# Optimization experiments

Measured on AMD Instinct MI355X. Metric: run time of the kernel, lower is better.

Reference implementation:

```python
import jax, jax.numpy as jnp
import numpy as np

NUM_HEADS = 16
ROPE_BASE = 10000.0


def apply_rope(x):
    # x: [B, T, H, D]; torchtune-style interleaved-pair RoPE, positions 0..T-1
    B, T, H, D = x.shape
    inv_freq = 1.0 / (ROPE_BASE ** (jnp.arange(0, D, 2, dtype=jnp.float32) / D))  # [D/2]
    pos = jnp.arange(T, dtype=jnp.float32)
    freqs = pos[:, None] * inv_freq[None, :]              # [T, D/2]
    cos = jnp.cos(freqs)[None, :, None, :].astype(x.dtype)
    sin = jnp.sin(freqs)[None, :, None, :].astype(x.dtype)
    x1 = x[..., 0::2]
    x2 = x[..., 1::2]
    o1 = x1 * cos - x2 * sin
    o2 = x2 * cos + x1 * sin
    return jnp.stack([o1, o2], axis=-1).reshape(B, T, H, D)


def setup_inputs() -> dict:
    key = jax.random.key(0)
    k1, k2, k3 = jax.random.split(key, 3)
    B, T, C = 2, 8192, 1024
    x = jax.random.normal(k1, (B, T, C), dtype=jnp.float32)
    # torch Linear weight layout [out_features, in_features]; fan-in scaling
    Wqkv = jax.random.normal(k2, (3 * C, C), dtype=jnp.float32) * (C ** -0.5)
    Wout = jax.random.normal(k3, (C, C), dtype=jnp.float32) * (C ** -0.5)
    return {"x": x, "Wqkv": Wqkv, "Wout": Wout}


def reference(x, Wqkv, Wout):
    B, T, C = x.shape
    H = NUM_HEADS
    D = C // H
    qkv = (x @ Wqkv.T).reshape(B, T, 3, H, D)
    q, k, v = qkv[:, :, 0], qkv[:, :, 1], qkv[:, :, 2]   # each [B, T, H, D]
    q = apply_rope(q)
    k = apply_rope(k)
    # Faithful to source: SDPA is called on [B, T, H, D] WITHOUT transposing,
    # so torch attends over the heads axis (L = H) with (B, T) as batch dims.
    scale = 1.0 / jnp.sqrt(jnp.asarray(D, dtype=x.dtype))
    scores = jnp.einsum('btqd,btkd->btqk', q, k) * scale  # [B, T, H, H]
    attn = jax.nn.softmax(scores, axis=-1)
    out = jnp.einsum('btqk,btkd->btqd', attn, v)          # [B, T, H, D]
    # Replicate attn_output.transpose(1, 2).contiguous().view(B, T, C)
    out = out.transpose(0, 2, 1, 3).reshape(B, T, C)
    return out @ Wout.T
```

## Files before the change

kernel.cpp:

```cpp
#include <hip/hip_runtime.h>
#include <stdint.h>

#define TT 8192
#define BT 16384
#define MCH 8192

typedef __attribute__((ext_vector_type(8))) __bf16 bf16x8;
typedef __attribute__((ext_vector_type(4))) __bf16 bf16x4;
typedef __attribute__((ext_vector_type(4))) short short4v;
typedef __attribute__((ext_vector_type(4))) float floatx4;

__device__ __forceinline__ float bf2f(unsigned short h) {
  union { unsigned u; float f; } x; x.u = ((unsigned)h) << 16; return x.f;
}
__device__ __forceinline__ unsigned short f2bf(float f) {
  union { float f; unsigned u; } x; x.f = f;
  unsigned r = (x.u + 0x7fffu + ((x.u >> 16) & 1u)) >> 16;
  return (unsigned short)r;
}
__device__ __forceinline__ void async16(const void* g, void* l) {
  __builtin_amdgcn_global_load_lds(
      (__attribute__((address_space(1))) void*)g,
      (__attribute__((address_space(3))) void*)l, 16, 0, 0);
}

__global__ __launch_bounds__(256) void cvt_f2b(
    const float* __restrict__ src, unsigned short* __restrict__ dst, int n4) {
  const int i = blockIdx.x * 256 + threadIdx.x;
  if (i < n4) {
    const float4 f = ((const float4*)src)[i];
    union { uint2 u2; unsigned short s[4]; } o;
    o.s[0] = f2bf(f.x); o.s[1] = f2bf(f.y);
    o.s[2] = f2bf(f.z); o.s[3] = f2bf(f.w);
    ((uint2*)dst)[i] = o.u2;
  }
}

__global__ __launch_bounds__(256) void rope_table_k(float2* __restrict__ tab) {
  const int i = blockIdx.x * 256 + threadIdx.x;
  if (i < TT * 32) {
    const int t = i >> 5, p = i & 31;
    const float f = (float)t * exp2f((float)p * -0.41524101186092f);
    float s, c;
    sincosf(f, &s, &c);
    tab[i] = make_float2(c, s);
  }
}

template <bool CF32>
__global__ __launch_bounds__(512, 4) void gemm_k32(
    const unsigned short* __restrict__ A,
    const unsigned short* __restrict__ W,
    void* __restrict__ C,
    int M, int N, int K)
{
  __shared__ __align__(16) unsigned short sm[2][(256 + 128) * 32];

  const int tid  = threadIdx.x;
  const int lane = tid & 63;
  const int wid  = tid >> 6;
  const int wr   = wid >> 1;
  const int wc   = wid & 1;
  const int lm   = lane & 15;
  const int kg   = lane >> 4;
  const int cxor = (lm >> 1) & 3;

  const int nb  = N >> 7;
  const int cpx = (int)gridDim.x >> 3;
  const int bid = blockIdx.x;
  const int swz = (bid & 7) * cpx + (bid >> 3);
  const int bm  = swz / nb;
  const int bn  = swz % nb;

  const int NT = K >> 5;

  const int sr  = lane >> 2;
  const int scb = lane & 3;
  const unsigned short* gsrc0;
  const unsigned short* gsrc1;
  const unsigned short* gsrc2;
  {
    const int r0 = wid * 16 + sr;
    const int r1 = 128 + r0;
    const int rB = wid * 16 + sr;
    gsrc0 = A + (size_t)(bm * 256 + r0) * (size_t)K + ((scb ^ ((r0 >> 1) & 3)) << 3);
    gsrc1 = A + (size_t)(bm * 256 + r1) * (size_t)K + ((scb ^ ((r1 >> 1) & 3)) << 3);
    gsrc2 = W + (size_t)(bn * 128 + rB) * (size_t)K + ((scb ^ ((rB >> 1) & 3)) << 3);
  }
  const int ld0 = wid * 1024;
  const int ld1 = 8192 + wid * 1024;
  const int ld2 = 16384 + wid * 1024;

  auto stage_tile = [&](int tt) {
    char* lb = (char*)sm[tt & 1];
    const size_t koff = (size_t)tt << 5;
    async16(gsrc0 + koff, lb + ld0);
    async16(gsrc1 + koff, lb + ld1);
    async16(gsrc2 + koff, lb + ld2);
  };

  floatx4 acc[4][4];
  floatx4 z = {0.f, 0.f, 0.f, 0.f};
#pragma unroll
  for (int i = 0; i < 4; ++i)
#pragma unroll
    for (int j = 0; j < 4; ++j) acc[i][j] = z;

  stage_tile(0);
  stage_tile(1);
  asm volatile("s_waitcnt vmcnt(3)" ::: "memory");
  __builtin_amdgcn_s_barrier();
  __builtin_amdgcn_sched_barrier(0);

  for (int t = 0; t < NT; ++t) {
    const unsigned short* Ab = sm[t & 1];
    const unsigned short* Bb = Ab + 256 * 32;

    bf16x8 af[4], bfr[4];
#pragma unroll
    for (int i = 0; i < 4; ++i) {
      const int rr = wr * 64 + i * 16 + lm;
      af[i] = *(const bf16x8*)(Ab + rr * 32 + ((kg ^ cxor) << 3));
    }
#pragma unroll
    for (int j = 0; j < 4; ++j) {
      const int rr = wc * 64 + j * 16 + lm;
      bfr[j] = *(const bf16x8*)(Bb + rr * 32 + ((kg ^ cxor) << 3));
    }

    __builtin_amdgcn_s_barrier();
    asm volatile("s_waitcnt lgkmcnt(0)" ::: "memory");
    __builtin_amdgcn_sched_barrier(0);

    if (t + 2 < NT) stage_tile(t + 2);

    __builtin_amdgcn_s_setprio(1);
#pragma unroll
    for (int i = 0; i < 4; ++i)
#pragma unroll
      for (int j = 0; j < 4; ++j)
        acc[i][j] = __builtin_amdgcn_mfma_f32_16x16x32_bf16(
            af[i], bfr[j], acc[i][j], 0, 0, 0);
    __builtin_amdgcn_s_setprio(0);

    if (t + 1 < NT) {
      if (t + 2 < NT)
        asm volatile("s_waitcnt vmcnt(3)" ::: "memory");
      else
        asm volatile("s_waitcnt vmcnt(0)" ::: "memory");
      __builtin_amdgcn_s_barrier();
      __builtin_amdgcn_sched_barrier(0);
    }
  }

#pragma unroll
  for (int i = 0; i < 4; ++i) {
    const int row0 = bm * 256 + wr * 64 + i * 16 + kg * 4;
#pragma unroll
    for (int j = 0; j < 4; ++j) {
      const int col = bn * 128 + wc * 64 + j * 16 + lm;
#pragma unroll
      for (int r = 0; r < 4; ++r) {
        if (CF32)
          ((float*)C)[(size_t)(row0 + r) * N + col] = acc[i][j][r];
        else
          ((unsigned short*)C)[(size_t)(row0 + r) * N + col] = f2bf(acc[i][j][r]);
      }
    }
  }
}

#if defined(__has_builtin)
#if __has_builtin(__builtin_amdgcn_mfma_f32_16x16x16_bf16)
#define PV_MFMA 1
#define PV_MFMA_CALL(a, b, c) __builtin_amdgcn_mfma_f32_16x16x16_bf16( \
    *(bf16x4*)&(a), *(bf16x4*)&(b), (c), 0, 0, 0)
#elif __has_builtin(__builtin_amdgcn_mfma_f32_16x16x16bf16_1k)
#define PV_MFMA 1
#define PV_MFMA_CALL(a, b, c) __builtin_amdgcn_mfma_f32_16x16x16bf16_1k( \
    (a), (b), (c), 0, 0, 0)
#else
#define PV_MFMA 0
#endif
#else
#define PV_MFMA 0
#endif

__global__ __launch_bounds__(128) void attn_rope_k(
    const unsigned short* __restrict__ qkv,
    const float2* __restrict__ tab,
    unsigned short* __restrict__ Y,
    int base)
{
  __shared__ __align__(16) unsigned short sQKV[2][3 * 16 * 72];
#if !PV_MFMA
  __shared__ float sP[2][256];
#endif

  const int wave = threadIdx.x >> 6;
  const int lane = threadIdx.x & 63;
  const int ml = blockIdx.x * 2 + wave;
  const int m  = base + ml;
  const int t  = m & (TT - 1);
  const int b  = m >> 13;

  unsigned short* QB = sQKV[wave];
  unsigned short* KB = QB + 16 * 72;
  unsigned short* VB = QB + 2 * 16 * 72;

  const int lm   = lane & 15;
  const int quad = lane >> 4;

  const uint4* row = (const uint4*)(qkv + (size_t)ml * 3072);
#pragma unroll
  for (int i = 0; i < 6; ++i) {
    const int c = lane + 64 * i;
    union { uint4 u4; unsigned short s[8]; } cv;
    cv.u4 = row[c];
    const int n0   = c * 8;
    const int part = n0 >> 10;
    const int h    = (n0 >> 6) & 15;
    const int d0   = n0 & 63;
    if (part < 2) {
      float f[8];
#pragma unroll
      for (int j = 0; j < 8; ++j) f[j] = bf2f(cv.s[j]);
      const int p0 = d0 >> 1;
      const float4 csA = *(const float4*)(tab + (t << 5) + p0);
      const float4 csB = *(const float4*)(tab + (t << 5) + p0 + 2);
      const float cs[4] = {csA.x, csA.z, csB.x, csB.z};
      const float sn[4] = {csA.y, csA.w, csB.y, csB.w};
#pragma unroll
      for (int j = 0; j < 4; ++j) {
        const float x1 = f[2 * j], x2 = f[2 * j + 1];
        cv.s[2 * j]     = f2bf(x1 * cs[j] - x2 * sn[j]);
        cv.s[2 * j + 1] = f2bf(x2 * cs[j] + x1 * sn[j]);
      }
    }
    unsigned short* dst = QB + part * (16 * 72) + h * 72 + d0;
    *(uint4*)dst = cv.u4;
  }
  __syncthreads();

  floatx4 accS = {0.f, 0.f, 0.f, 0.f};
#pragma unroll
  for (int half = 0; half < 2; ++half) {
    const bf16x8 kf = *(const bf16x8*)(KB + lm * 72 + half * 32 + quad * 8);
    const bf16x8 qf = *(const bf16x8*)(QB + lm * 72 + half * 32 + quad * 8);
    accS = __builtin_amdgcn_mfma_f32_16x16x32_bf16(kf, qf, accS, 0, 0, 0);
  }
  float s4[4];
  float mx = -1e30f;
#pragma unroll
  for (int j = 0; j < 4; ++j) { s4[j] = accS[j] * 0.125f; mx = fmaxf(mx, s4[j]); }
  mx = fmaxf(mx, __shfl_xor(mx, 16, 64));
  mx = fmaxf(mx, __shfl_xor(mx, 32, 64));
  float sum = 0.f;
#pragma unroll
  for (int j = 0; j < 4; ++j) { s4[j] = __expf(s4[j] - mx); sum += s4[j]; }
  sum += __shfl_xor(sum, 16, 64);
  sum += __shfl_xor(sum, 32, 64);
  const float inv = 1.0f / sum;

#if PV_MFMA
  union { short4v v; unsigned short s[4]; } pf;
#pragma unroll
  for (int j = 0; j < 4; ++j) pf.s[j] = s4[j] * inv == 0.f ? 0 : f2bf(s4[j] * inv);
#pragma unroll
  for (int dtile = 0; dtile < 4; ++dtile) {
    union { short4v v; unsigned short s[4]; } vf;
#pragma unroll
    for (int j = 0; j < 4; ++j)
      vf.s[j] = VB[(quad * 4 + j) * 72 + dtile * 16 + lm];
    floatx4 accO = {0.f, 0.f, 0.f, 0.f};
    accO = PV_MFMA_CALL(pf.v, vf.v, accO);
    const int col = (t & 15) * 64 + dtile * 16 + lm;
#pragma unroll
    for (int r = 0; r < 4; ++r) {
      const size_t rr = (size_t)b * TT + (size_t)(quad * 4 + r) * 512 + (t >> 4);
      Y[rr * 1024 + col] = f2bf(accO[r]);
    }
  }
#else
  float* P = sP[wave];
#pragma unroll
  for (int j = 0; j < 4; ++j) P[(quad * 4 + j) * 16 + lm] = s4[j] * inv;
  __syncthreads();
  float o[16];
#pragma unroll
  for (int dd = 0; dd < 16; ++dd) o[dd] = 0.f;
#pragma unroll
  for (int kh = 0; kh < 16; ++kh) {
    const float a = P[kh * 16 + lm];
    union { uint4 u4; unsigned short s[8]; } v0, v1;
    v0.u4 = *(const uint4*)(VB + kh * 72 + quad * 16);
    v1.u4 = *(const uint4*)(VB + kh * 72 + quad * 16 + 8);
#pragma unroll
    for (int dd = 0; dd < 8; ++dd) {
      o[dd]     += a * bf2f(v0.s[dd]);
      o[dd + 8] += a * bf2f(v1.s[dd]);
    }
  }
  const size_t rr = (size_t)b * TT + (size_t)lm * 512 + (t >> 4);
  unsigned short* yp = Y + rr * 1024 + (t & 15) * 64 + quad * 16;
  union { uint4 u4; unsigned short s[8]; } o1, o2;
#pragma unroll
  for (int dd = 0; dd < 8; ++dd) o1.s[dd] = f2bf(o[dd]);
#pragma unroll
  for (int dd = 0; dd < 8; ++dd) o2.s[dd] = f2bf(o[8 + dd]);
  ((uint4*)yp)[0] = o1.u4;
  ((uint4*)yp)[1] = o2.u4;
#endif
}

extern "C" void kernel_launch(void* const* d_in, const int* in_sizes, int n_in,
                              void* d_out, int out_size, void* d_ws, size_t ws_size,
                              hipStream_t stream) {
  const float* x    = (const float*)d_in[0];
  const float* Wqkv = (const float*)d_in[1];
  const float* Wout = (const float*)d_in[2];
  float* out = (float*)d_out;

  unsigned short* Y     = (unsigned short*)d_ws;
  unsigned short* Wqkvb = Y + (size_t)BT * 1024;
  unsigned short* Woutb = Wqkvb + (size_t)3072 * 1024;
  unsigned short* xb    = Woutb + (size_t)1024 * 1024;
  unsigned short* qkvC  = (unsigned short*)d_out;
  float2* tab           = (float2*)((char*)d_out + (size_t)52 * 1024 * 1024);

  rope_table_k<<<dim3(TT * 32 / 256), dim3(256), 0, stream>>>(tab);
  cvt_f2b<<<dim3(3072 * 1024 / 4 / 256), dim3(256), 0, stream>>>(Wqkv, Wqkvb, 3072 * 1024 / 4);
  cvt_f2b<<<dim3(1024 * 1024 / 4 / 256), dim3(256), 0, stream>>>(Wout, Woutb, 1024 * 1024 / 4);

  for (int base = 0; base < BT; base += MCH) {
    cvt_f2b<<<dim3(MCH * 1024 / 4 / 256), dim3(256), 0, stream>>>(
        x + (size_t)base * 1024, xb, MCH * 1024 / 4);
    gemm_k32<false><<<dim3((MCH / 256) * (3072 / 128)), dim3(512), 0, stream>>>(
        xb, Wqkvb, qkvC, MCH, 3072, 1024);
    attn_rope_k<<<dim3(MCH / 2), dim3(128), 0, stream>>>(qkvC, tab, Y, base);
  }

  gemm_k32<true><<<dim3((BT / 256) * (1024 / 128)), dim3(512), 0, stream>>>(
      Y, Woutb, out, BT, 1024, 1024);
}
```

Measured before the change: 311.7 us.

## Rework GEMM into 4-wave, triple-buffered pipeline with prefetched A fragments

Replaces the 8-wave, double-buffered GEMM with a 4-wave kernel in which each wave computes a 128x64 sub-tile. LDS is now triple-buffered so global loads run two tiles ahead, and A fragments for the next k-step are read from LDS while the current MFMAs execute, using alternating register sets. The aim is to hide global and LDS latency and raise MFMA density per wave. The cost is roughly double the accumulator registers, lower occupancy (launch bounds 256,2) and more LDS per block. The unrolled pair loop also assumes NT is even.

```diff
diff --git a/kernel.cpp b/kernel.cpp
--- a/kernel.cpp
+++ b/kernel.cpp
@@ -48,13 +48,13 @@
 }
 
 template <bool CF32>
-__global__ __launch_bounds__(512, 4) void gemm_k32(
+__global__ __launch_bounds__(256, 2) void gemm_p3(
     const unsigned short* __restrict__ A,
     const unsigned short* __restrict__ W,
     void* __restrict__ C,
     int M, int N, int K)
 {
-  __shared__ __align__(16) unsigned short sm[2][(256 + 128) * 32];
+  __shared__ __align__(16) unsigned short sm[3][(256 + 128) * 32];
 
   const int tid  = threadIdx.x;
   const int lane = tid & 63;
@@ -76,86 +76,106 @@
 
   const int sr  = lane >> 2;
   const int scb = lane & 3;
-  const unsigned short* gsrc0;
-  const unsigned short* gsrc1;
-  const unsigned short* gsrc2;
-  {
-    const int r0 = wid * 16 + sr;
-    const int r1 = 128 + r0;
-    const int rB = wid * 16 + sr;
-    gsrc0 = A + (size_t)(bm * 256 + r0) * (size_t)K + ((scb ^ ((r0 >> 1) & 3)) << 3);
-    gsrc1 = A + (size_t)(bm * 256 + r1) * (size_t)K + ((scb ^ ((r1 >> 1) & 3)) << 3);
-    gsrc2 = W + (size_t)(bn * 128 + rB) * (size_t)K + ((scb ^ ((rB >> 1) & 3)) << 3);
-  }
-  const int ld0 = wid * 1024;
-  const int ld1 = 8192 + wid * 1024;
-  const int ld2 = 16384 + wid * 1024;
-
-  auto stage_tile = [&](int tt) {
-    char* lb = (char*)sm[tt & 1];
+  const unsigned short* gA[4];
+  const unsigned short* gB[2];
+#pragma unroll
+  for (int q = 0; q < 4; ++q) {
+    const int r = (wid * 4 + q) * 16 + sr;
+    gA[q] = A + (size_t)(bm * 256 + r) * (size_t)K + ((scb ^ ((r >> 1) & 3)) << 3);
+  }
+#pragma unroll
+  for (int q = 0; q < 2; ++q) {
+    const int r = (wid * 2 + q) * 16 + sr;
+    gB[q] = W + (size_t)(bn * 128 + r) * (size_t)K + ((scb ^ ((r >> 1) & 3)) << 3);
+  }
+
+  auto stage_tile = [&](int tt, unsigned short* lb) {
     const size_t koff = (size_t)tt << 5;
-    async16(gsrc0 + koff, lb + ld0);
-    async16(gsrc1 + koff, lb + ld1);
-    async16(gsrc2 + koff, lb + ld2);
+    char* lc = (char*)lb;
+#pragma unroll
+    for (int q = 0; q < 4; ++q)
+      async16(gA[q] + koff, lc + (wid * 4 + q) * 1024);
+#pragma unroll
+    for (int q = 0; q < 2; ++q)
+      async16(gB[q] + koff, lc + 16384 + (wid * 2 + q) * 1024);
   };
 
-  floatx4 acc[4][4];
+  auto readA = [&](const unsigned short* buf, bf16x8* dst) {
+#pragma unroll
+    for (int i = 0; i < 8; ++i) {
+      const int rr = wr * 128 + i * 16 + lm;
+      dst[i] = *(const bf16x8*)(buf + rr * 32 + ((kg ^ cxor) << 3));
+    }
+  };
+  auto readB = [&](const unsigned short* buf, bf16x8* dst) {
+#pragma unroll
+    for (int j = 0; j < 4; ++j) {
+      const int rr = wc * 64 + j * 16 + lm;
+      dst[j] = *(const bf16x8*)(buf + 256 * 32 + rr * 32 + ((kg ^ cxor) << 3));
+    }
+  };
+
+  floatx4 acc[8][4];
   floatx4 z = {0.f, 0.f, 0.f, 0.f};
 #pragma unroll
-  for (int i = 0; i < 4; ++i)
+  for (int i = 0; i < 8; ++i)
 #pragma unroll
     for (int j = 0; j < 4; ++j) acc[i][j] = z;
 
-  stage_tile(0);
-  stage_tile(1);
-  asm volatile("s_waitcnt vmcnt(3)" ::: "memory");
+  unsigned short* b0 = sm[0];
+  unsigned short* b1 = sm[1];
+  unsigned short* b2 = sm[2];
+
+  stage_tile(0, b0);
+  stage_tile(1, b1);
+  stage_tile(2, b2);
+  asm volatile("s_waitcnt vmcnt(6)" ::: "memory");
   __builtin_amdgcn_s_barrier();
   __builtin_amdgcn_sched_barrier(0);
 
-  for (int t = 0; t < NT; ++t) {
-    const unsigned short* Ab = sm[t & 1];
-    const unsigned short* Bb = Ab + 256 * 32;
-
-    bf16x8 af[4], bfr[4];
-#pragma unroll
-    for (int i = 0; i < 4; ++i) {
-      const int rr = wr * 64 + i * 16 + lm;
-      af[i] = *(const bf16x8*)(Ab + rr * 32 + ((kg ^ cxor) << 3));
-    }
-#pragma unroll
-    for (int j = 0; j < 4; ++j) {
-      const int rr = wc * 64 + j * 16 + lm;
-      bfr[j] = *(const bf16x8*)(Bb + rr * 32 + ((kg ^ cxor) << 3));
-    }
-
-    __builtin_amdgcn_s_barrier();
-    asm volatile("s_waitcnt lgkmcnt(0)" ::: "memory");
-    __builtin_amdgcn_sched_barrier(0);
-
-    if (t + 2 < NT) stage_tile(t + 2);
-
-    __builtin_amdgcn_s_setprio(1);
-#pragma unroll
-    for (int i = 0; i < 4; ++i)
-#pragma unroll
-      for (int j = 0; j < 4; ++j)
-        acc[i][j] = __builtin_amdgcn_mfma_f32_16x16x32_bf16(
-            af[i], bfr[j], acc[i][j], 0, 0, 0);
-    __builtin_amdgcn_s_setprio(0);
-
-    if (t + 1 < NT) {
-      if (t + 2 < NT)
-        asm volatile("s_waitcnt vmcnt(3)" ::: "memory");
-      else
-        asm volatile("s_waitcnt vmcnt(0)" ::: "memory");
-      __builtin_amdgcn_s_barrier();
-      __builtin_amdgcn_sched_barrier(0);
-    }
-  }
-
-#pragma unroll
-  for (int i = 0; i < 4; ++i) {
-    const int row0 = bm * 256 + wr * 64 + i * 16 + kg * 4;
+  bf16x8 afA[8], afB[8], bfr[4];
+  readA(b0, afA);
+
+#define SUBITER(U, CUR, NXT)                                                  \
+  {                                                                           \
+    const int u_ = (U);                                                       \
+    readB(b0, bfr);                                                           \
+    __builtin_amdgcn_sched_barrier(0);   \
+    if (u_ + 1 < NT) {                                                        \
+      readA(b1, NXT);                                                         \
+      asm volatile("s_waitcnt lgkmcnt(8)" ::: "memory");                      \
+    } else {                                                                  \
+      asm volatile("s_waitcnt lgkmcnt(0)" ::: "memory");                      \
+    }                                                                         \
+    __builtin_amdgcn_sched_barrier(0);                                        \
+    __builtin_amdgcn_s_barrier();              \
+    if (u_ + 3 < NT) stage_tile(u_ + 3, b0);                                  \
+    __builtin_amdgcn_s_setprio(1);                                            \
+    _Pragma("unroll")                                                         \
+    for (int i = 0; i < 8; ++i)                                               \
+      _Pragma("unroll")                                                       \
+      for (int j = 0; j < 4; ++j)                                             \
+        acc[i][j] = __builtin_amdgcn_mfma_f32_16x16x32_bf16(                  \
+            CUR[i], bfr[j], acc[i][j], 0, 0, 0);                              \
+    __builtin_amdgcn_s_setprio(0);                                            \
+    if (u_ + 4 <= NT)                                                         \
+      asm volatile("s_waitcnt vmcnt(6)" ::: "memory");                        \
+    else                                                                      \
+      asm volatile("s_waitcnt vmcnt(0)" ::: "memory");                        \
+    __builtin_amdgcn_sched_barrier(0);                                        \
+    __builtin_amdgcn_s_barrier();                                             \
+    unsigned short* tmp_ = b0; b0 = b1; b1 = b2; b2 = tmp_;                   \
+  }
+
+  for (int u = 0; u < NT; u += 2) {
+    SUBITER(u, afA, afB);
+    SUBITER(u + 1, afB, afA);
+  }
+#undef SUBITER
+
+#pragma unroll
+  for (int i = 0; i < 8; ++i) {
+    const int row0 = bm * 256 + wr * 128 + i * 16 + kg * 4;
 #pragma unroll
     for (int j = 0; j < 4; ++j) {
       const int col = bn * 128 + wc * 64 + j * 16 + lm;
@@ -335,11 +355,11 @@
   for (int base = 0; base < BT; base += MCH) {
     cvt_f2b<<<dim3(MCH * 1024 / 4 / 256), dim3(256), 0, stream>>>(
         x + (size_t)base * 1024, xb, MCH * 1024 / 4);
-    gemm_k32<false><<<dim3((MCH / 256) * (3072 / 128)), dim3(512), 0, stream>>>(
+    gemm_p3<false><<<dim3((MCH / 256) * (3072 / 128)), dim3(256), 0, stream>>>(
         xb, Wqkvb, qkvC, MCH, 3072, 1024);
     attn_rope_k<<<dim3(MCH / 2), dim3(128), 0, stream>>>(qkvC, tab, Y, base);
   }
 
-  gemm_k32<true><<<dim3((BT / 256) * (1024 / 128)), dim3(512), 0, stream>>>(
+  gemm_p3<true><<<dim3((BT / 256) * (1024 / 128)), dim3(256), 0, stream>>>(
       Y, Woutb, out, BT, 1024, 1024);
 }
```

Measured after the change: 307.5 us. Within noise of the previous version (-1.3%).
